# Kernel optimization log

Measured on AMD Instinct MI355X. Metric: run time of the kernel, lower is better.

## Reference

```python
import jax, jax.numpy as jnp
import numpy as np

N = 50000; E = 800000; F_IN = 128; H = 16; G = 256
DIMS = [F_IN, H, 2 * H, 4 * H, 4 * H, 8 * H]
EPS = 1e-5


def setup_inputs() -> dict:
    key = jax.random.key(0)
    ks = iter(jax.random.split(key, 40))
    inp = {}
    inp["x"] = jax.random.normal(next(ks), (N, F_IN), dtype=jnp.float32)
    inp["edge_index"] = jax.random.randint(next(ks), (2, E), 0, N, dtype=jnp.int32)
    inp["edge_weight"] = jax.random.uniform(next(ks), (E,), dtype=jnp.float32)
    inp["batch"] = jnp.sort(jax.random.randint(next(ks), (N,), 0, G, dtype=jnp.int32))
    for i in range(5):
        din, dout = DIMS[i], DIMS[i + 1]
        inp[f"W{i+1}"] = jax.random.normal(next(ks), (din, dout), dtype=jnp.float32) / np.sqrt(din).astype(np.float32)
        inp[f"b{i+1}"] = jnp.zeros((dout,), jnp.float32)
        inp[f"g{i+1}"] = jnp.ones((dout,), jnp.float32)
        inp[f"bt{i+1}"] = jnp.zeros((dout,), jnp.float32)
    inp["fc1_w"] = jax.random.normal(next(ks), (8 * H, 4 * H), dtype=jnp.float32) / np.sqrt(8 * H).astype(np.float32)
    inp["fc1_b"] = jnp.zeros((4 * H,), jnp.float32)
    inp["fc2_w"] = jax.random.normal(next(ks), (4 * H, 1), dtype=jnp.float32) / np.sqrt(4 * H).astype(np.float32)
    inp["fc2_b"] = jnp.zeros((1,), jnp.float32)
    return inp


def _gcn_norm(edge_index, edge_weight, n):
    # PyG GCNConv: add self-loops (weight 1), symmetric deg^-1/2 normalization.
    loop = jnp.arange(n, dtype=edge_index.dtype)
    row = jnp.concatenate([edge_index[0], loop])  # source
    col = jnp.concatenate([edge_index[1], loop])  # target
    w = jnp.concatenate([edge_weight, jnp.ones((n,), edge_weight.dtype)])
    deg = jax.ops.segment_sum(w, col, num_segments=n)
    dis = jnp.where(deg > 0, jax.lax.rsqrt(jnp.maximum(deg, 1e-12)), 0.0)
    return row, col, dis[row] * w * dis[col]


def _bn(h, g, b):
    # BatchNorm1d, training-mode batch statistics (biased variance, eps=1e-5)
    mu = h.mean(0)
    v = h.var(0)
    return g * (h - mu) * jax.lax.rsqrt(v + EPS) + b


def reference(x, edge_index, edge_weight, batch,
              W1, b1, g1, bt1, W2, b2, g2, bt2, W3, b3, g3, bt3,
              W4, b4, g4, bt4, W5, b5, g5, bt5,
              fc1_w, fc1_b, fc2_w, fc2_b):
    n = x.shape[0]
    row, col, norm = _gcn_norm(edge_index, edge_weight, n)

    def conv(h, W, b):
        m = h @ W                                   # [N, dout] dense transform
        agg = jax.ops.segment_sum(m[row] * norm[:, None], col, num_segments=n)
        return agg + b

    h = _bn(jax.nn.relu(conv(x, W1, b1)), g1, bt1)
    h = _bn(jax.nn.relu(conv(h, W2, b2)), g2, bt2)
    h = _bn(jax.nn.relu(conv(h, W3, b3)), g3, bt3)
    h = jax.nn.relu(_bn(conv(h, W4, b4), g4, bt4))   # layer4: conv->bn->relu
    h = _bn(conv(h, W5, b5), g5, bt5)                # layer5: conv->bn
    pooled = jax.ops.segment_sum(h, batch, num_segments=G)  # global_add_pool -> [G, 8H]
    p = jax.nn.relu(pooled)
    p = jax.nn.relu(p @ fc1_w + fc1_b)
    # dropout is identity in eval mode
    return (p @ fc2_w + fc2_b).reshape(-1)          # [G]
```

## Files before the change

kernel.cpp:

```cpp
#include <hip/hip_runtime.h>

#define NN 50000
#define NE 800000
#define NG 256
#define NBUCKET 16
#define PARTSZ (NBUCKET * 256)

#define NBKT 391
#define ABLK 391
#define ASLICE 2048
#define BCAP 2560

__device__ __forceinline__ float bf2f(unsigned short u) {
    return __uint_as_float(((unsigned)u) << 16);
}
__device__ __forceinline__ unsigned short f2bf(float f) {
    unsigned b = __float_as_uint(f);
    return (unsigned short)((b + 0x7FFF + ((b >> 16) & 1)) >> 16);
}

__global__ void k_init(float* part) {
    int i = blockIdx.x * blockDim.x + threadIdx.x;
    if (i < 5 * PARTSZ) part[i] = 0.f;
}

__global__ void kA1(const int* __restrict__ col, int* __restrict__ bb, int e) {
    __shared__ int cnt[NBKT];
    for (int j = threadIdx.x; j < NBKT; j += 256) cnt[j] = 0;
    __syncthreads();
    int start = blockIdx.x * ASLICE;
    int end = min(start + ASLICE, e);
    for (int i = start + threadIdx.x; i < end; i += 256)
        atomicAdd(&cnt[col[i] >> 7], 1);
    __syncthreads();
    for (int j = threadIdx.x; j < NBKT; j += 256) bb[blockIdx.x * NBKT + j] = cnt[j];
}

__global__ void kA2a(int* __restrict__ bb, int* __restrict__ totals) {
    __shared__ int v[ABLK];
    int k = blockIdx.x;
    for (int b = threadIdx.x; b < ABLK; b += 256) v[b] = bb[b * NBKT + k];
    __syncthreads();
    if (threadIdx.x == 0) {
        int run = 0;
        for (int b = 0; b < ABLK; ++b) { int t = v[b]; v[b] = run; run += t; }
        totals[k] = run;
    }
    __syncthreads();
    for (int b = threadIdx.x; b < ABLK; b += 256) bb[b * NBKT + k] = v[b];
}

__global__ void kA2b(const int* __restrict__ totals, int* __restrict__ bucketbase) {
    __shared__ int v[NBKT];
    for (int j = threadIdx.x; j < NBKT; j += 256) v[j] = totals[j];
    __syncthreads();
    if (threadIdx.x == 0) {
        int run = 0;
        for (int k = 0; k < NBKT; ++k) { int t = v[k]; v[k] = run; run += t; }
        bucketbase[NBKT] = run;
    }
    __syncthreads();
    for (int j = threadIdx.x; j < NBKT; j += 256) bucketbase[j] = v[j];
}

__global__ void kA3(const int* __restrict__ row, const int* __restrict__ col,
                    const float* __restrict__ ew, const int* __restrict__ bb,
                    const int* __restrict__ bucketbase, int2* __restrict__ staging, int e) {
    __shared__ int cur[NBKT];
    for (int j = threadIdx.x; j < NBKT; j += 256)
        cur[j] = bucketbase[j] + bb[blockIdx.x * NBKT + j];
    __syncthreads();
    int start = blockIdx.x * ASLICE;
    int end = min(start + ASLICE, e);
    for (int i = start + threadIdx.x; i < end; i += 256) {
        int c = col[i];
        int p = atomicAdd(&cur[c >> 7], 1);
        staging[p] = make_int2(row[i] | ((c & 127) << 16), __float_as_int(ew[i]));
    }
}

__global__ void __launch_bounds__(256) kB(const int* __restrict__ bucketbase,
                                          const int2* __restrict__ staging,
                                          int2* __restrict__ csr, int* __restrict__ ptr,
                                          float* __restrict__ dis, int n) {
    __shared__ int2 st[BCAP];
    __shared__ int2 outb[BCAP];
    __shared__ int hist[129];
    __shared__ int cur[128];
    int k = blockIdx.x, t = threadIdx.x;
    int base = bucketbase[k], cnt = bucketbase[k + 1] - base;
    int node0 = k << 7;
    int ncov = min(128, n - node0);
    if (t < 129) hist[t] = 0;
    __syncthreads();
    if (cnt <= BCAP) {
        for (int i = t; i < cnt; i += 256) {
            int2 v = staging[base + i];
            st[i] = v;
            atomicAdd(&hist[v.x >> 16], 1);
        }
        __syncthreads();
        if (t == 0) {
            int run = 0;
            for (int j = 0; j < 128; ++j) { int h = hist[j]; hist[j] = run; run += h; }
            hist[128] = run;
        }
        __syncthreads();
        if (t < 128) cur[t] = hist[t];
        if (t < ncov) ptr[node0 + t] = base + hist[t];
        __syncthreads();
        for (int i = t; i < cnt; i += 256) {
            int2 v = st[i];
            int j = v.x >> 16;
            int p = atomicAdd(&cur[j], 1);
            outb[p] = make_int2(v.x & 0xFFFF, v.y);
        }
        __syncthreads();
        for (int i = t; i < cnt; i += 256) csr[base + i] = outb[i];
        if (t < ncov) {
            float s = 1.f;
            int a = hist[t], b2 = hist[t + 1];
            for (int p = a; p < b2; ++p) s += __int_as_float(outb[p].y);
            dis[node0 + t] = rsqrtf(s);
        }
    } else {
        for (int i = t; i < cnt; i += 256) atomicAdd(&hist[staging[base + i].x >> 16], 1);
        __syncthreads();
        if (t == 0) {
            int run = 0;
            for (int j = 0; j < 128; ++j) { int h = hist[j]; hist[j] = run; run += h; }
            hist[128] = run;
        }
        __syncthreads();
        if (t < 128) cur[t] = hist[t];
        if (t < ncov) ptr[node0 + t] = base + hist[t];
        __syncthreads();
        for (int i = t; i < cnt; i += 256) {
            int2 v = staging[base + i];
            int j = v.x >> 16;
            int p = atomicAdd(&cur[j], 1);
            csr[base + p] = make_int2(v.x & 0xFFFF, v.y);
        }
        __threadfence_block();
        __syncthreads();
        if (t < ncov) {
            float s = 1.f;
            int a = hist[t], b2 = hist[t + 1];
            for (int p = a; p < b2; ++p) s += __int_as_float(csr[base + p].y);
            dis[node0 + t] = rsqrtf(s);
        }
    }
    if (k == gridDim.x - 1 && t == 0) ptr[n] = bucketbase[NBKT];
}

__global__ void k_scale(const int* __restrict__ ptr, int2* __restrict__ csr,
                        const float* __restrict__ dis, int n) {
    int i = blockIdx.x * blockDim.x + threadIdx.x;
    if (i >= n) return;
    float dc = dis[i];
    int p1 = ptr[i + 1];
    for (int p = ptr[i]; p < p1; ++p) {
        int2 v = csr[p];
        v.y = __float_as_int(dis[v.x] * __int_as_float(v.y) * dc);
        csr[p] = v;
    }
}

template <int D, int BF16>
__device__ __forceinline__ float4 load_row(const void* src, int node, int l4) {
    if (BF16) {
        const unsigned short* sb = (const unsigned short*)src;
        ushort4 r = *(const ushort4*)(sb + (size_t)node * D + (l4 << 2));
        float4 f;
        f.x = bf2f(r.x); f.y = bf2f(r.y); f.z = bf2f(r.z); f.w = bf2f(r.w);
        return f;
    } else {
        const float4* s4 = (const float4*)src;
        return s4[(size_t)node * (D / 4) + l4];
    }
}

template <int D, int EP, int POSTAFF, int PREAFF, int EPI, int BF16IN>
__global__ void k_gather(const void* __restrict__ src, const int* __restrict__ ptr,
                         const int2* __restrict__ csr, const float* __restrict__ dis,
                         const float* __restrict__ partIn, const float* __restrict__ gmv,
                         const float* __restrict__ btv,
                         const float* __restrict__ bias, float* __restrict__ partOut,
                         float* __restrict__ out, int n) {
    const int TPN = D / 4;
    const int LPN = TPN * EP;
    const int CONSUME = POSTAFF || PREAFF;
    __shared__ float ls[EPI ? D : 1], lq[EPI ? D : 1];
    __shared__ float scs[CONSUME ? D : 4], shs[CONSUME ? D : 4];
    int tid = threadIdx.x;
    if (EPI && tid < D) { ls[tid] = 0.f; lq[tid] = 0.f; }
    if (CONSUME && tid < D) {
        float s = 0.f, q = 0.f;
#pragma unroll
        for (int b2 = 0; b2 < NBUCKET; ++b2) {
            s += partIn[b2 * 256 + tid];
            q += partIn[b2 * 256 + 128 + tid];
        }
        float mu = s / (float)n;
        float var = q / (float)n - mu * mu;
        float a = gmv[tid] * rsqrtf(var + 1e-5f);
        scs[tid] = a;
        shs[tid] = btv[tid] - mu * a;
    }
    if (EPI || CONSUME) __syncthreads();

    int t = blockIdx.x * blockDim.x + tid;
    int node = t / LPN;
    int r = t - node * LPN;
    int e0 = r / TPN;
    int l4 = r - e0 * TPN;
    bool valid = node < n;
    int nc = valid ? node : n - 1;

    float4 sc = {0,0,0,0}, sh = {0,0,0,0};
    if (CONSUME) {
        sc = ((const float4*)scs)[l4];
        sh = ((const float4*)shs)[l4];
    }
    float4 acc = {0.f, 0.f, 0.f, 0.f};
    float sumw = 0.f;
    if (e0 == 0) {
        float d = dis[nc];
        float w0 = d * d;
        float4 v = load_row<D, BF16IN>(src, nc, l4);
        if (PREAFF) {
            v.x = fmaxf(sc.x * v.x + sh.x, 0.f); v.y = fmaxf(sc.y * v.y + sh.y, 0.f);
            v.z = fmaxf(sc.z * v.z + sh.z, 0.f); v.w = fmaxf(sc.w * v.w + sh.w, 0.f);
        }
        acc.x = w0 * v.x; acc.y = w0 * v.y; acc.z = w0 * v.z; acc.w = w0 * v.w;
        sumw = w0;
    }
    int p0 = ptr[nc], p1 = ptr[nc + 1];
    int p = p0 + e0;
    for (; p + 3 * EP < p1; p += 4 * EP) {
        int2 c0 = csr[p], c1 = csr[p + EP], c2 = csr[p + 2 * EP], c3 = csr[p + 3 * EP];
        float e0w = __int_as_float(c0.y), e1w = __int_as_float(c1.y);
        float e2w = __int_as_float(c2.y), e3w = __int_as_float(c3.y);
        float4 u0 = load_row<D, BF16IN>(src, c0.x, l4);
        float4 u1 = load_row<D, BF16IN>(src, c1.x, l4);
        float4 u2 = load_row<D, BF16IN>(src, c2.x, l4);
        float4 u3 = load_row<D, BF16IN>(src, c3.x, l4);
        if (PREAFF) {
            u0.x = fmaxf(sc.x*u0.x+sh.x,0.f); u0.y = fmaxf(sc.y*u0.y+sh.y,0.f);
            u0.z = fmaxf(sc.z*u0.z+sh.z,0.f); u0.w = fmaxf(sc.w*u0.w+sh.w,0.f);
            u1.x = fmaxf(sc.x*u1.x+sh.x,0.f); u1.y = fmaxf(sc.y*u1.y+sh.y,0.f);
            u1.z = fmaxf(sc.z*u1.z+sh.z,0.f); u1.w = fmaxf(sc.w*u1.w+sh.w,0.f);
            u2.x = fmaxf(sc.x*u2.x+sh.x,0.f); u2.y = fmaxf(sc.y*u2.y+sh.y,0.f);
            u2.z = fmaxf(sc.z*u2.z+sh.z,0.f); u2.w = fmaxf(sc.w*u2.w+sh.w,0.f);
            u3.x = fmaxf(sc.x*u3.x+sh.x,0.f); u3.y = fmaxf(sc.y*u3.y+sh.y,0.f);
            u3.z = fmaxf(sc.z*u3.z+sh.z,0.f); u3.w = fmaxf(sc.w*u3.w+sh.w,0.f);
        }
        acc.x += e0w*u0.x + e1w*u1.x + e2w*u2.x + e3w*u3.x;
        acc.y += e0w*u0.y + e1w*u1.y + e2w*u2.y + e3w*u3.y;
        acc.z += e0w*u0.z + e1w*u1.z + e2w*u2.z + e3w*u3.z;
        acc.w += e0w*u0.w + e1w*u1.w + e2w*u2.w + e3w*u3.w;
        if (POSTAFF) sumw += e0w + e1w + e2w + e3w;
    }
    for (; p < p1; p += EP) {
        int2 ce = csr[p];
        float w = __int_as_float(ce.y);
        float4 u = load_row<D, BF16IN>(src, ce.x, l4);
        if (PREAFF) {
            u.x = fmaxf(sc.x*u.x+sh.x,0.f); u.y = fmaxf(sc.y*u.y+sh.y,0.f);
            u.z = fmaxf(sc.z*u.z+sh.z,0.f); u.w = fmaxf(sc.w*u.w+sh.w,0.f);
        }
        acc.x += w*u.x; acc.y += w*u.y; acc.z += w*u.z; acc.w += w*u.w;
        if (POSTAFF) sumw += w;
    }
    if (EP > 1) {
#pragma unroll
        for (int off = TPN; off < LPN; off <<= 1) {
            acc.x += __shfl_xor(acc.x, off, 64);
            acc.y += __shfl_xor(acc.y, off, 64);
            acc.z += __shfl_xor(acc.z, off, 64);
            acc.w += __shfl_xor(acc.w, off, 64);
            if (POSTAFF) sumw += __shfl_xor(sumw, off, 64);
        }
    }
    if (POSTAFF) {
        acc.x = sc.x * acc.x + sh.x * sumw;
        acc.y = sc.y * acc.y + sh.y * sumw;
        acc.z = sc.z * acc.z + sh.z * sumw;
        acc.w = sc.w * acc.w + sh.w * sumw;
    }
    if (EPI) {
        float4 b = ((const float4*)bias)[l4];
        acc.x = fmaxf(acc.x + b.x, 0.f);
        acc.y = fmaxf(acc.y + b.y, 0.f);
        acc.z = fmaxf(acc.z + b.z, 0.f);
        acc.w = fmaxf(acc.w + b.w, 0.f);
        if (valid) ((float4*)out)[nc * TPN + l4] = acc;
        float s0 = valid ? acc.x : 0.f, s1 = valid ? acc.y : 0.f;
        float s2 = valid ? acc.z : 0.f, s3 = valid ? acc.w : 0.f;
        float q0 = s0*s0, q1 = s1*s1, q2 = s2*s2, q3 = s3*s3;
        for (int off = TPN; off < 64; off <<= 1) {
            s0 += __shfl_down(s0, off, 64); s1 += __shfl_down(s1, off, 64);
            s2 += __shfl_down(s2, off, 64); s3 += __shfl_down(s3, off, 64);
            q0 += __shfl_down(q0, off, 64); q1 += __shfl_down(q1, off, 64);
            q2 += __shfl_down(q2, off, 64); q3 += __shfl_down(q3, off, 64);
        }
        int lane = tid & 63;
        if (lane < TPN) {
            atomicAdd(&ls[4*lane+0], s0); atomicAdd(&ls[4*lane+1], s1);
            atomicAdd(&ls[4*lane+2], s2); atomicAdd(&ls[4*lane+3], s3);
            atomicAdd(&lq[4*lane+0], q0); atomicAdd(&lq[4*lane+1], q1);
            atomicAdd(&lq[4*lane+2], q2); atomicAdd(&lq[4*lane+3], q3);
        }
        __syncthreads();
        int bkt = (blockIdx.x & (NBUCKET - 1)) * 256;
        if (tid < D) {
            atomicAdd(&partOut[bkt + tid], ls[tid]);
            atomicAdd(&partOut[bkt + 128 + tid], lq[tid]);
        }
    } else {
        if (valid && e0 == 0) ((float4*)out)[nc * TPN + l4] = acc;
    }
}

template <int DIN, int DOUT, int RELU, int EPI, int NPT, int BF16OUT>
__global__ void k_gemm(const float* __restrict__ h, const float* __restrict__ W,
                       const float* __restrict__ bias, float* __restrict__ partOut,
                       void* __restrict__ m, int n) {
    const int TPN = DOUT / 4;
    const int GPB = 256 / TPN;
    __shared__ float Wl[DIN * DOUT];
    __shared__ float ls[EPI ? DOUT : 1], lq[EPI ? DOUT : 1];
    int tid = threadIdx.x;
    for (int i = tid; i < DIN * DOUT / 4; i += 256)
        ((float4*)Wl)[i] = ((const float4*)W)[i];
    if (EPI && tid < DOUT) { ls[tid] = 0.f; lq[tid] = 0.f; }
    __syncthreads();

    int jq = tid % TPN;
    int group = tid / TPN;
    int node0 = (blockIdx.x * GPB + group) * NPT;
    const float4* h4 = (const float4*)h;
    int hb[NPT];
    bool val[NPT];
#pragma unroll
    for (int i = 0; i < NPT; ++i) {
        int nd = node0 + i;
        val[i] = nd < n;
        hb[i] = (val[i] ? nd : n - 1) * (DIN / 4);
    }
    float4 acc[NPT];
#pragma unroll
    for (int i = 0; i < NPT; ++i) acc[i] = {0.f, 0.f, 0.f, 0.f};

#pragma unroll 4
    for (int k4 = 0; k4 < DIN / 4; ++k4) {
        const float* wb = &Wl[(k4 * 4) * DOUT + jq * 4];
        float4 w0 = *(const float4*)(wb);
        float4 w1 = *(const float4*)(wb + DOUT);
        float4 w2 = *(const float4*)(wb + 2 * DOUT);
        float4 w3 = *(const float4*)(wb + 3 * DOUT);
#pragma unroll
        for (int i = 0; i < NPT; ++i) {
            float4 hv = h4[hb[i] + k4];
            acc[i].x += hv.x*w0.x + hv.y*w1.x + hv.z*w2.x + hv.w*w3.x;
            acc[i].y += hv.x*w0.y + hv.y*w1.y + hv.z*w2.y + hv.w*w3.y;
            acc[i].z += hv.x*w0.z + hv.y*w1.z + hv.z*w2.z + hv.w*w3.z;
            acc[i].w += hv.x*w0.w + hv.y*w1.w + hv.z*w2.w + hv.w*w3.w;
        }
    }

    float4 bv = {0,0,0,0};
    if (EPI) bv = ((const float4*)bias)[jq];
    float4 sv = {0,0,0,0}, qv = {0,0,0,0};
#pragma unroll
    for (int i = 0; i < NPT; ++i) {
        float4 a = acc[i];
        if (EPI) {
            a.x += bv.x; a.y += bv.y; a.z += bv.z; a.w += bv.w;
            if (RELU) {
                a.x = fmaxf(a.x, 0.f); a.y = fmaxf(a.y, 0.f);
                a.z = fmaxf(a.z, 0.f); a.w = fmaxf(a.w, 0.f);
            }
        }
        if (val[i]) {
            if (BF16OUT) {
                ushort4 o;
                o.x = f2bf(a.x); o.y = f2bf(a.y); o.z = f2bf(a.z); o.w = f2bf(a.w);
                *(ushort4*)((unsigned short*)m + (size_t)(node0 + i) * DOUT + (jq << 2)) = o;
            } else {
                ((float4*)m)[(size_t)(node0 + i) * TPN + jq] = a;
            }
            if (EPI) {
                sv.x += a.x; sv.y += a.y; sv.z += a.z; sv.w += a.w;
                qv.x += a.x*a.x; qv.y += a.y*a.y; qv.z += a.z*a.z; qv.w += a.w*a.w;
            }
        }
    }
    if (EPI) {
        for (int off = TPN; off < 64; off <<= 1) {
            sv.x += __shfl_down(sv.x, off, 64); sv.y += __shfl_down(sv.y, off, 64);
            sv.z += __shfl_down(sv.z, off, 64); sv.w += __shfl_down(sv.w, off, 64);
            qv.x += __shfl_down(qv.x, off, 64); qv.y += __shfl_down(qv.y, off, 64);
            qv.z += __shfl_down(qv.z, off, 64); qv.w += __shfl_down(qv.w, off, 64);
        }
        int lane = tid & 63;
        if (lane < TPN) {
            atomicAdd(&ls[4*lane+0], sv.x); atomicAdd(&ls[4*lane+1], sv.y);
            atomicAdd(&ls[4*lane+2], sv.z); atomicAdd(&ls[4*lane+3], sv.w);
            atomicAdd(&lq[4*lane+0], qv.x); atomicAdd(&lq[4*lane+1], qv.y);
            atomicAdd(&lq[4*lane+2], qv.z); atomicAdd(&lq[4*lane+3], qv.w);
        }
        __syncthreads();
        int bkt = (blockIdx.x & (NBUCKET - 1)) * 256;
        if (tid < DOUT) {
            atomicAdd(&partOut[bkt + tid], ls[tid]);
            atomicAdd(&partOut[bkt + 128 + tid], lq[tid]);
        }
    }
}

__global__ void k_poolhead(const float* __restrict__ h, const int* __restrict__ batch,
                           const float* __restrict__ partIn, const float* __restrict__ gmv,
                           const float* __restrict__ btv,
                           const float* __restrict__ fc1w, const float* __restrict__ fc1b,
                           const float* __restrict__ fc2w, const float* __restrict__ fc2b,
                           float* __restrict__ out, int n) {
    __shared__ float tmp[256];
    __shared__ float pl[128];
    __shared__ float scs[128], shs[128];
    int g = blockIdx.x;
    int tid = threadIdx.x;
    if (tid < 128) {
        float s = 0.f, q = 0.f;
#pragma unroll
        for (int b2 = 0; b2 < NBUCKET; ++b2) {
            s += partIn[b2 * 256 + tid];
            q += partIn[b2 * 256 + 128 + tid];
        }
        float mu = s / (float)n;
        float var = q / (float)n - mu * mu;
        float a = gmv[tid] * rsqrtf(var + 1e-5f);
        scs[tid] = a;
        shs[tid] = btv[tid] - mu * a;
    }
    int j = tid & 127, prt = tid >> 7;
    int a = 0, b = n;
    while (a < b) { int mid = (a + b) >> 1; if (batch[mid] < g) a = mid + 1; else b = mid; }
    int lo = a;
    b = n;
    while (a < b) { int mid = (a + b) >> 1; if (batch[mid] < g + 1) a = mid + 1; else b = mid; }
    int hi = a;

    float acc = 0.f;
    for (int node = lo + prt; node < hi; node += 2) acc += h[(long)node * 128 + j];
    tmp[tid] = acc;
    __syncthreads();
    if (tid < 128) {
        float cnt = (float)(hi - lo);
        float p = scs[tid] * (tmp[tid] + tmp[tid + 128]) + shs[tid] * cnt;
        pl[tid] = fmaxf(p, 0.f);
    }
    __syncthreads();
    if (tid < 64) {
        float v1 = fc1b[tid];
        for (int k = 0; k < 128; ++k) v1 += pl[k] * fc1w[k * 64 + tid];
        v1 = fmaxf(v1, 0.f);
        float v = v1 * fc2w[tid];
        for (int off = 32; off > 0; off >>= 1) v += __shfl_down(v, off, 64);
        if (tid == 0) out[g] = v + fc2b[0];
    }
}

extern "C" void kernel_launch(void* const* d_in, const int* in_sizes, int n_in,
                              void* d_out, int out_size, void* d_ws, size_t ws_size,
                              hipStream_t stream) {
    const float* x     = (const float*)d_in[0];
    const int*   ei    = (const int*)d_in[1];
    const float* ew    = (const float*)d_in[2];
    const int*   batch = (const int*)d_in[3];
    const float *W[5], *b[5], *gm[5], *bt[5];
    for (int i = 0; i < 5; ++i) {
        W[i]  = (const float*)d_in[4 + 4 * i];
        b[i]  = (const float*)d_in[5 + 4 * i];
        gm[i] = (const float*)d_in[6 + 4 * i];
        bt[i] = (const float*)d_in[7 + 4 * i];
    }
    const float* fc1w = (const float*)d_in[24];
    const float* fc1b = (const float*)d_in[25];
    const float* fc2w = (const float*)d_in[26];
    const float* fc2b = (const float*)d_in[27];
    float* out = (float*)d_out;

    char* wsb = (char*)d_ws;
    float* dis    = (float*)wsb;  wsb += sizeof(float) * NN;
    int*   ptr    = (int*)wsb;    wsb += sizeof(int) * (NN + 4);
    int*   bb     = (int*)wsb;    wsb += sizeof(int) * ABLK * NBKT;
    int*   totals = (int*)wsb;    wsb += sizeof(int) * (NBKT + 1);
    int*   bbase  = (int*)wsb;    wsb += sizeof(int) * (NBKT + 3);
    int2*  staging= (int2*)wsb;   wsb += sizeof(int2) * NE;
    int2*  csr    = (int2*)wsb;   wsb += sizeof(int2) * NE;
    float* part   = (float*)wsb;  wsb += sizeof(float) * 5 * PARTSZ;
    unsigned short* bufB = (unsigned short*)wsb;  wsb += sizeof(unsigned short) * (size_t)NN * 64;
    float* buf1   = (float*)wsb;  wsb += sizeof(float) * (long)NN * 128;
    float* buf2   = (float*)wsb;  wsb += sizeof(float) * (long)NN * 128;

    const int* row = ei;
    const int* col = ei + NE;
    const int B = 256;
    const int NB_N = (NN + B - 1) / B;

    k_init<<<(5 * PARTSZ + B - 1) / B, B, 0, stream>>>(part);
    kA1<<<ABLK, B, 0, stream>>>(col, bb, NE);
    kA2a<<<NBKT, B, 0, stream>>>(bb, totals);
    kA2b<<<1, B, 0, stream>>>(totals, bbase);
    kA3<<<ABLK, B, 0, stream>>>(row, col, ew, bb, bbase, staging, NE);
    kB<<<NBKT, B, 0, stream>>>(bbase, staging, csr, ptr, dis, NN);
    k_scale<<<NB_N, B, 0, stream>>>(ptr, csr, dis, NN);

    auto grid4 = [](long threads) { return (int)((threads + 255) / 256); };
    auto ggrid = [](int npb) { return (NN + npb - 1) / npb; };

    k_gemm<128, 16, 0, 0, 2, 0><<<ggrid((256/4)*2), B, 0, stream>>>(x, W[0], b[0], nullptr, buf1, NN);
    k_gather<16, 1, 0, 0, 1, 0><<<grid4((long)NN * 4), B, 0, stream>>>(buf1, ptr, csr, dis,
                                                                       nullptr, nullptr, nullptr,
                                                                       b[0], part + 0 * PARTSZ, buf2, NN);

    k_gather<16, 1, 1, 0, 0, 0><<<grid4((long)NN * 4), B, 0, stream>>>(buf2, ptr, csr, dis,
                                                                       part + 0 * PARTSZ, gm[0], bt[0],
                                                                       nullptr, nullptr, buf1, NN);
    k_gemm<16, 32, 1, 1, 4, 1><<<ggrid((256/8)*4), B, 0, stream>>>(buf1, W[1], b[1], part + 1 * PARTSZ, bufB, NN);

    k_gather<32, 4, 1, 0, 0, 1><<<grid4((long)NN * 32), B, 0, stream>>>(bufB, ptr, csr, dis,
                                                                        part + 1 * PARTSZ, gm[1], bt[1],
                                                                        nullptr, nullptr, buf1, NN);
    k_gemm<32, 64, 1, 1, 4, 1><<<ggrid((256/16)*4), B, 0, stream>>>(buf1, W[2], b[2], part + 2 * PARTSZ, bufB, NN);

    k_gather<64, 4, 1, 0, 0, 1><<<grid4((long)NN * 64), B, 0, stream>>>(bufB, ptr, csr, dis,
                                                                        part + 2 * PARTSZ, gm[2], bt[2],
                                                                        nullptr, nullptr, buf1, NN);
    k_gemm<64, 64, 0, 1, 4, 1><<<ggrid((256/16)*4), B, 0, stream>>>(buf1, W[3], b[3], part + 3 * PARTSZ, bufB, NN);

    k_gather<64, 4, 0, 1, 0, 1><<<grid4((long)NN * 64), B, 0, stream>>>(bufB, ptr, csr, dis,
                                                                        part + 3 * PARTSZ, gm[3], bt[3],
                                                                        nullptr, nullptr, buf1, NN);
    k_gemm<64, 128, 0, 1, 4, 0><<<ggrid((256/32)*4), B, 0, stream>>>(buf1, W[4], b[4], part + 4 * PARTSZ, buf2, NN);

    k_poolhead<<<NG, 256, 0, stream>>>(buf2, batch, part + 4 * PARTSZ, gm[4], bt[4],
                                       fc1w, fc1b, fc2w, fc2b, out, NN);
}
```

Measured before the change: 426.0 us.

## Fuse gather and dense transform per layer, fold edge scaling into first gather

Layers 2-5 now run as one kernel each: a block aggregates 16 nodes' neighbour rows into shared memory, then applies the weight matrix from shared memory, so the intermediate aggregated features no longer round-trip through global memory. The separate edge-weight normalisation pass is folded into the first-layer gather, which writes the normalised weights back into the CSR array. Zeroing of the statistics buffer moves into the histogram kernel, removing two launches. The trade-off is 16-node blocks with a large shared weight tile, which may lower occupancy and repeat the weight load in every block.

```diff
diff --git a/kernel.cpp b/kernel.cpp
--- a/kernel.cpp
+++ b/kernel.cpp
@@ -1,4 +1,5 @@
 #include <hip/hip_runtime.h>
+#include <stdint.h>
 
 #define NN 50000
 #define NE 800000
@@ -19,14 +20,10 @@
     return (unsigned short)((b + 0x7FFF + ((b >> 16) & 1)) >> 16);
 }
 
-__global__ void k_init(float* part) {
-    int i = blockIdx.x * blockDim.x + threadIdx.x;
-    if (i < 5 * PARTSZ) part[i] = 0.f;
-}
-
-__global__ void kA1(const int* __restrict__ col, int* __restrict__ bb, int e) {
+__global__ void kA1(const int* __restrict__ col, int* __restrict__ bb, float* part, int e) {
     __shared__ int cnt[NBKT];
     for (int j = threadIdx.x; j < NBKT; j += 256) cnt[j] = 0;
+    for (int i = blockIdx.x * 256 + threadIdx.x; i < 5 * PARTSZ; i += ABLK * 256) part[i] = 0.f;
     __syncthreads();
     int start = blockIdx.x * ASLICE;
     int end = min(start + ASLICE, e);
@@ -153,16 +150,121 @@
     if (k == gridDim.x - 1 && t == 0) ptr[n] = bucketbase[NBKT];
 }
 
-__global__ void k_scale(const int* __restrict__ ptr, int2* __restrict__ csr,
-                        const float* __restrict__ dis, int n) {
-    int i = blockIdx.x * blockDim.x + threadIdx.x;
-    if (i >= n) return;
-    float dc = dis[i];
-    int p1 = ptr[i + 1];
-    for (int p = ptr[i]; p < p1; ++p) {
-        int2 v = csr[p];
-        v.y = __float_as_int(dis[v.x] * __int_as_float(v.y) * dc);
-        csr[p] = v;
+__global__ void k_gemm1(const float* __restrict__ h, const float* __restrict__ W,
+                        float* __restrict__ m, int n) {
+    __shared__ float Wl[128 * 16];
+    int tid = threadIdx.x;
+    for (int i = tid; i < 128 * 16 / 4; i += 256)
+        ((float4*)Wl)[i] = ((const float4*)W)[i];
+    __syncthreads();
+    int jq = tid % 4, group = tid / 4;
+    int node0 = (blockIdx.x * 64 + group) * 2;
+    const float4* h4 = (const float4*)h;
+    int hb[2]; bool val[2];
+#pragma unroll
+    for (int i = 0; i < 2; ++i) {
+        int nd = node0 + i;
+        val[i] = nd < n;
+        hb[i] = (val[i] ? nd : n - 1) * 32;
+    }
+    float4 acc[2];
+    acc[0] = {0,0,0,0}; acc[1] = {0,0,0,0};
+#pragma unroll 4
+    for (int k4 = 0; k4 < 32; ++k4) {
+        const float* wb = &Wl[(k4 * 4) * 16 + jq * 4];
+        float4 w0 = *(const float4*)(wb);
+        float4 w1 = *(const float4*)(wb + 16);
+        float4 w2 = *(const float4*)(wb + 32);
+        float4 w3 = *(const float4*)(wb + 48);
+#pragma unroll
+        for (int i = 0; i < 2; ++i) {
+            float4 hv = h4[hb[i] + k4];
+            acc[i].x += hv.x*w0.x + hv.y*w1.x + hv.z*w2.x + hv.w*w3.x;
+            acc[i].y += hv.x*w0.y + hv.y*w1.y + hv.z*w2.y + hv.w*w3.y;
+            acc[i].z += hv.x*w0.z + hv.y*w1.z + hv.z*w2.z + hv.w*w3.z;
+            acc[i].w += hv.x*w0.w + hv.y*w1.w + hv.z*w2.w + hv.w*w3.w;
+        }
+    }
+#pragma unroll
+    for (int i = 0; i < 2; ++i)
+        if (val[i]) ((float4*)m)[(node0 + i) * 4 + jq] = acc[i];
+}
+
+__global__ void k_l1gather(const float* __restrict__ src, const int* __restrict__ ptr,
+                           int2* __restrict__ csr, const float* __restrict__ dis,
+                           const float* __restrict__ bias, float* __restrict__ partOut,
+                           float* __restrict__ out, int n) {
+    __shared__ float ls[16], lq[16];
+    int tid = threadIdx.x;
+    if (tid < 16) { ls[tid] = 0.f; lq[tid] = 0.f; }
+    __syncthreads();
+    int t = blockIdx.x * 256 + tid;
+    int node = t >> 2;
+    int l4 = t & 3;
+    bool valid = node < n;
+    int nc = valid ? node : n - 1;
+    const float4* s4 = (const float4*)src;
+    float dc = dis[nc];
+    float w0 = dc * dc;
+    float4 v = s4[nc * 4 + l4];
+    float4 acc = { w0 * v.x, w0 * v.y, w0 * v.z, w0 * v.w };
+    int p0 = ptr[nc], p1 = ptr[nc + 1];
+    int p = p0;
+    for (; p + 4 <= p1; p += 4) {
+        int2 c0 = csr[p], c1 = csr[p+1], c2 = csr[p+2], c3 = csr[p+3];
+        float e0 = dis[c0.x] * __int_as_float(c0.y) * dc;
+        float e1 = dis[c1.x] * __int_as_float(c1.y) * dc;
+        float e2 = dis[c2.x] * __int_as_float(c2.y) * dc;
+        float e3 = dis[c3.x] * __int_as_float(c3.y) * dc;
+        float4 u0 = s4[c0.x * 4 + l4];
+        float4 u1 = s4[c1.x * 4 + l4];
+        float4 u2 = s4[c2.x * 4 + l4];
+        float4 u3 = s4[c3.x * 4 + l4];
+        acc.x += e0*u0.x + e1*u1.x + e2*u2.x + e3*u3.x;
+        acc.y += e0*u0.y + e1*u1.y + e2*u2.y + e3*u3.y;
+        acc.z += e0*u0.z + e1*u1.z + e2*u2.z + e3*u3.z;
+        acc.w += e0*u0.w + e1*u1.w + e2*u2.w + e3*u3.w;
+        if (l4 == 0) {
+            csr[p]   = make_int2(c0.x, __float_as_int(e0));
+            csr[p+1] = make_int2(c1.x, __float_as_int(e1));
+            csr[p+2] = make_int2(c2.x, __float_as_int(e2));
+            csr[p+3] = make_int2(c3.x, __float_as_int(e3));
+        }
+    }
+    for (; p < p1; ++p) {
+        int2 ce = csr[p];
+        float w = dis[ce.x] * __int_as_float(ce.y) * dc;
+        float4 u = s4[ce.x * 4 + l4];
+        acc.x += w*u.x; acc.y += w*u.y; acc.z += w*u.z; acc.w += w*u.w;
+        if (l4 == 0) csr[p] = make_int2(ce.x, __float_as_int(w));
+    }
+    float4 b = ((const float4*)bias)[l4];
+    acc.x = fmaxf(acc.x + b.x, 0.f);
+    acc.y = fmaxf(acc.y + b.y, 0.f);
+    acc.z = fmaxf(acc.z + b.z, 0.f);
+    acc.w = fmaxf(acc.w + b.w, 0.f);
+    if (valid) ((float4*)out)[nc * 4 + l4] = acc;
+    float s0 = valid ? acc.x : 0.f, s1 = valid ? acc.y : 0.f;
+    float s2 = valid ? acc.z : 0.f, s3 = valid ? acc.w : 0.f;
+    float q0 = s0*s0, q1 = s1*s1, q2 = s2*s2, q3 = s3*s3;
+    for (int off = 4; off < 64; off <<= 1) {
+        s0 += __shfl_down(s0, off, 64); s1 += __shfl_down(s1, off, 64);
+        s2 += __shfl_down(s2, off, 64); s3 += __shfl_down(s3, off, 64);
+        q0 += __shfl_down(q0, off, 64); q1 += __shfl_down(q1, off, 64);
+        q2 += __shfl_down(q2, off, 64); q3 += __shfl_down(q3, off, 64);
+    }
+    int lane = tid & 63;
+    if (lane < 4) {
+        atomicAdd(&ls[4*lane+0], s0); atomicAdd(&ls[4*lane+1], s1);
+        atomicAdd(&ls[4*lane+2], s2); atomicAdd(&ls[4*lane+3], s3);
+        atomicAdd(&lq[4*lane+0], q0); atomicAdd(&lq[4*lane+1], q1);
+        atomicAdd(&lq[4*lane+2], q2); atomicAdd(&lq[4*lane+3], q3);
+    }
+    __syncthreads();
+    int bkt = (blockIdx.x & (NBUCKET - 1)) * 256;
+    if (tid < 16) {
+        atomicAdd(&partOut[bkt + tid], ls[tid]);
+        atomicAdd(&partOut[bkt + 128 + tid], lq[tid]);
     }
 }
 
@@ -180,21 +282,26 @@
     }
 }
 
-template <int D, int EP, int POSTAFF, int PREAFF, int EPI, int BF16IN>
-__global__ void k_gather(const void* __restrict__ src, const int* __restrict__ ptr,
-                         const int2* __restrict__ csr, const float* __restrict__ dis,
-                         const float* __restrict__ partIn, const float* __restrict__ gmv,
-                         const float* __restrict__ btv,
-                         const float* __restrict__ bias, float* __restrict__ partOut,
-                         float* __restrict__ out, int n) {
-    const int TPN = D / 4;
-    const int LPN = TPN * EP;
-    const int CONSUME = POSTAFF || PREAFF;
-    __shared__ float ls[EPI ? D : 1], lq[EPI ? D : 1];
-    __shared__ float scs[CONSUME ? D : 4], shs[CONSUME ? D : 4];
+template <int DIN, int DOUT, int EP, int POSTAFF, int PREAFF, int RELU,
+          int BF16IN, int BF16OUT, int NPB>
+__global__ void __launch_bounds__(256) k_fused(
+        const void* __restrict__ src, const int* __restrict__ ptr,
+        const int2* __restrict__ csr, const float* __restrict__ dis,
+        const float* __restrict__ partIn, const float* __restrict__ gmv,
+        const float* __restrict__ btv, const float* __restrict__ W,
+        const float* __restrict__ bias, float* __restrict__ partOut,
+        void* __restrict__ out, int n) {
+    const int TPN1 = DIN / 4, LPN = TPN1 * EP, GN1 = 256 / LPN;
+    const int TPN2 = DOUT / 4, G2 = 256 / TPN2;
+    const int HS = DIN + 4;
+    __shared__ float Wl[DIN * DOUT];
+    __shared__ float hrow[NPB * HS];
+    __shared__ float scs[DIN], shs[DIN];
+    __shared__ float ls[DOUT], lq[DOUT];
     int tid = threadIdx.x;
-    if (EPI && tid < D) { ls[tid] = 0.f; lq[tid] = 0.f; }
-    if (CONSUME && tid < D) {
+    for (int i = tid; i < DIN * DOUT / 4; i += 256)
+        ((float4*)Wl)[i] = ((const float4*)W)[i];
+    if (tid < DIN) {
         float s = 0.f, q = 0.f;
 #pragma unroll
         for (int b2 = 0; b2 < NBUCKET; ++b2) {
@@ -207,204 +314,134 @@
         scs[tid] = a;
         shs[tid] = btv[tid] - mu * a;
     }
-    if (EPI || CONSUME) __syncthreads();
-
-    int t = blockIdx.x * blockDim.x + tid;
-    int node = t / LPN;
-    int r = t - node * LPN;
-    int e0 = r / TPN;
-    int l4 = r - e0 * TPN;
-    bool valid = node < n;
-    int nc = valid ? node : n - 1;
-
-    float4 sc = {0,0,0,0}, sh = {0,0,0,0};
-    if (CONSUME) {
-        sc = ((const float4*)scs)[l4];
-        sh = ((const float4*)shs)[l4];
-    }
-    float4 acc = {0.f, 0.f, 0.f, 0.f};
-    float sumw = 0.f;
-    if (e0 == 0) {
-        float d = dis[nc];
-        float w0 = d * d;
-        float4 v = load_row<D, BF16IN>(src, nc, l4);
-        if (PREAFF) {
-            v.x = fmaxf(sc.x * v.x + sh.x, 0.f); v.y = fmaxf(sc.y * v.y + sh.y, 0.f);
-            v.z = fmaxf(sc.z * v.z + sh.z, 0.f); v.w = fmaxf(sc.w * v.w + sh.w, 0.f);
-        }
-        acc.x = w0 * v.x; acc.y = w0 * v.y; acc.z = w0 * v.z; acc.w = w0 * v.w;
-        sumw = w0;
-    }
-    int p0 = ptr[nc], p1 = ptr[nc + 1];
-    int p = p0 + e0;
-    for (; p + 3 * EP < p1; p += 4 * EP) {
-        int2 c0 = csr[p], c1 = csr[p + EP], c2 = csr[p + 2 * EP], c3 = csr[p + 3 * EP];
-        float e0w = __int_as_float(c0.y), e1w = __int_as_float(c1.y);
-        float e2w = __int_as_float(c2.y), e3w = __int_as_float(c3.y);
-        float4 u0 = load_row<D, BF16IN>(src, c0.x, l4);
-        float4 u1 = load_row<D, BF16IN>(src, c1.x, l4);
-        float4 u2 = load_row<D, BF16IN>(src, c2.x, l4);
-        float4 u3 = load_row<D, BF16IN>(src, c3.x, l4);
-        if (PREAFF) {
-            u0.x = fmaxf(sc.x*u0.x+sh.x,0.f); u0.y = fmaxf(sc.y*u0.y+sh.y,0.f);
-            u0.z = fmaxf(sc.z*u0.z+sh.z,0.f); u0.w = fmaxf(sc.w*u0.w+sh.w,0.f);
-            u1.x = fmaxf(sc.x*u1.x+sh.x,0.f); u1.y = fmaxf(sc.y*u1.y+sh.y,0.f);
-            u1.z = fmaxf(sc.z*u1.z+sh.z,0.f); u1.w = fmaxf(sc.w*u1.w+sh.w,0.f);
-            u2.x = fmaxf(sc.x*u2.x+sh.x,0.f); u2.y = fmaxf(sc.y*u2.y+sh.y,0.f);
-            u2.z = fmaxf(sc.z*u2.z+sh.z,0.f); u2.w = fmaxf(sc.w*u2.w+sh.w,0.f);
-            u3.x = fmaxf(sc.x*u3.x+sh.x,0.f); u3.y = fmaxf(sc.y*u3.y+sh.y,0.f);
-            u3.z = fmaxf(sc.z*u3.z+sh.z,0.f); u3.w = fmaxf(sc.w*u3.w+sh.w,0.f);
-        }
-        acc.x += e0w*u0.x + e1w*u1.x + e2w*u2.x + e3w*u3.x;
-        acc.y += e0w*u0.y + e1w*u1.y + e2w*u2.y + e3w*u3.y;
-        acc.z += e0w*u0.z + e1w*u1.z + e2w*u2.z + e3w*u3.z;
-        acc.w += e0w*u0.w + e1w*u1.w + e2w*u2.w + e3w*u3.w;
-        if (POSTAFF) sumw += e0w + e1w + e2w + e3w;
-    }
-    for (; p < p1; p += EP) {
-        int2 ce = csr[p];
-        float w = __int_as_float(ce.y);
-        float4 u = load_row<D, BF16IN>(src, ce.x, l4);
-        if (PREAFF) {
-            u.x = fmaxf(sc.x*u.x+sh.x,0.f); u.y = fmaxf(sc.y*u.y+sh.y,0.f);
-            u.z = fmaxf(sc.z*u.z+sh.z,0.f); u.w = fmaxf(sc.w*u.w+sh.w,0.f);
-        }
-        acc.x += w*u.x; acc.y += w*u.y; acc.z += w*u.z; acc.w += w*u.w;
-        if (POSTAFF) sumw += w;
-    }
-    if (EP > 1) {
-#pragma unroll
-        for (int off = TPN; off < LPN; off <<= 1) {
-            acc.x += __shfl_xor(acc.x, off, 64);
-            acc.y += __shfl_xor(acc.y, off, 64);
-            acc.z += __shfl_xor(acc.z, off, 64);
-            acc.w += __shfl_xor(acc.w, off, 64);
-            if (POSTAFF) sumw += __shfl_xor(sumw, off, 64);
-        }
-    }
-    if (POSTAFF) {
-        acc.x = sc.x * acc.x + sh.x * sumw;
-        acc.y = sc.y * acc.y + sh.y * sumw;
-        acc.z = sc.z * acc.z + sh.z * sumw;
-        acc.w = sc.w * acc.w + sh.w * sumw;
-    }
-    if (EPI) {
-        float4 b = ((const float4*)bias)[l4];
-        acc.x = fmaxf(acc.x + b.x, 0.f);
-        acc.y = fmaxf(acc.y + b.y, 0.f);
-        acc.z = fmaxf(acc.z + b.z, 0.f);
-        acc.w = fmaxf(acc.w + b.w, 0.f);
-        if (valid) ((float4*)out)[nc * TPN + l4] = acc;
-        float s0 = valid ? acc.x : 0.f, s1 = valid ? acc.y : 0.f;
-        float s2 = valid ? acc.z : 0.f, s3 = valid ? acc.w : 0.f;
-        float q0 = s0*s0, q1 = s1*s1, q2 = s2*s2, q3 = s3*s3;
-        for (int off = TPN; off < 64; off <<= 1) {
-            s0 += __shfl_down(s0, off, 64); s1 += __shfl_down(s1, off, 64);
-            s2 += __shfl_down(s2, off, 64); s3 += __shfl_down(s3, off, 64);
-            q0 += __shfl_down(q0, off, 64); q1 += __shfl_down(q1, off, 64);
-            q2 += __shfl_down(q2, off, 64); q3 += __shfl_down(q3, off, 64);
-        }
-        int lane = tid & 63;
-        if (lane < TPN) {
-            atomicAdd(&ls[4*lane+0], s0); atomicAdd(&ls[4*lane+1], s1);
-            atomicAdd(&ls[4*lane+2], s2); atomicAdd(&ls[4*lane+3], s3);
-            atomicAdd(&lq[4*lane+0], q0); atomicAdd(&lq[4*lane+1], q1);
-            atomicAdd(&lq[4*lane+2], q2); atomicAdd(&lq[4*lane+3], q3);
-        }
-        __syncthreads();
-        int bkt = (blockIdx.x & (NBUCKET - 1)) * 256;
-        if (tid < D) {
-            atomicAdd(&partOut[bkt + tid], ls[tid]);
-            atomicAdd(&partOut[bkt + 128 + tid], lq[tid]);
-        }
-    } else {
-        if (valid && e0 == 0) ((float4*)out)[nc * TPN + l4] = acc;
-    }
-}
-
-template <int DIN, int DOUT, int RELU, int EPI, int NPT, int BF16OUT>
-__global__ void k_gemm(const float* __restrict__ h, const float* __restrict__ W,
-                       const float* __restrict__ bias, float* __restrict__ partOut,
-                       void* __restrict__ m, int n) {
-    const int TPN = DOUT / 4;
-    const int GPB = 256 / TPN;
-    __shared__ float Wl[DIN * DOUT];
-    __shared__ float ls[EPI ? DOUT : 1], lq[EPI ? DOUT : 1];
-    int tid = threadIdx.x;
-    for (int i = tid; i < DIN * DOUT / 4; i += 256)
-        ((float4*)Wl)[i] = ((const float4*)W)[i];
-    if (EPI && tid < DOUT) { ls[tid] = 0.f; lq[tid] = 0.f; }
-    __syncthreads();
-
-    int jq = tid % TPN;
-    int group = tid / TPN;
-    int node0 = (blockIdx.x * GPB + group) * NPT;
-    const float4* h4 = (const float4*)h;
-    int hb[NPT];
-    bool val[NPT];
-#pragma unroll
-    for (int i = 0; i < NPT; ++i) {
-        int nd = node0 + i;
-        val[i] = nd < n;
-        hb[i] = (val[i] ? nd : n - 1) * (DIN / 4);
-    }
-    float4 acc[NPT];
-#pragma unroll
-    for (int i = 0; i < NPT; ++i) acc[i] = {0.f, 0.f, 0.f, 0.f};
-
-#pragma unroll 4
-    for (int k4 = 0; k4 < DIN / 4; ++k4) {
-        const float* wb = &Wl[(k4 * 4) * DOUT + jq * 4];
-        float4 w0 = *(const float4*)(wb);
-        float4 w1 = *(const float4*)(wb + DOUT);
-        float4 w2 = *(const float4*)(wb + 2 * DOUT);
-        float4 w3 = *(const float4*)(wb + 3 * DOUT);
-#pragma unroll
-        for (int i = 0; i < NPT; ++i) {
-            float4 hv = h4[hb[i] + k4];
-            acc[i].x += hv.x*w0.x + hv.y*w1.x + hv.z*w2.x + hv.w*w3.x;
-            acc[i].y += hv.x*w0.y + hv.y*w1.y + hv.z*w2.y + hv.w*w3.y;
-            acc[i].z += hv.x*w0.z + hv.y*w1.z + hv.z*w2.z + hv.w*w3.z;
-            acc[i].w += hv.x*w0.w + hv.y*w1.w + hv.z*w2.w + hv.w*w3.w;
-        }
-    }
-
-    float4 bv = {0,0,0,0};
-    if (EPI) bv = ((const float4*)bias)[jq];
-    float4 sv = {0,0,0,0}, qv = {0,0,0,0};
-#pragma unroll
-    for (int i = 0; i < NPT; ++i) {
-        float4 a = acc[i];
-        if (EPI) {
+    if (tid < DOUT) { ls[tid] = 0.f; lq[tid] = 0.f; }
+    __syncthreads();
+
+    int nodebase = blockIdx.x * NPB;
+    {
+        int grp = tid / LPN, r = tid % LPN;
+        int e0 = r / TPN1, l4 = r % TPN1;
+        float4 sc = ((const float4*)scs)[l4];
+        float4 sh = ((const float4*)shs)[l4];
+#pragma unroll
+        for (int pass = 0; pass < NPB / GN1; ++pass) {
+            int nl = pass * GN1 + grp;
+            int node = nodebase + nl;
+            int nc = node < n ? node : n - 1;
+            float4 acc = {0.f, 0.f, 0.f, 0.f};
+            float sumw = 0.f;
+            if (e0 == 0) {
+                float d = dis[nc];
+                float w0 = d * d;
+                float4 v = load_row<DIN, BF16IN>(src, nc, l4);
+                if (PREAFF) {
+                    v.x = fmaxf(sc.x*v.x+sh.x, 0.f); v.y = fmaxf(sc.y*v.y+sh.y, 0.f);
+                    v.z = fmaxf(sc.z*v.z+sh.z, 0.f); v.w = fmaxf(sc.w*v.w+sh.w, 0.f);
+                }
+                acc.x = w0*v.x; acc.y = w0*v.y; acc.z = w0*v.z; acc.w = w0*v.w;
+                sumw = w0;
+            }
+            int p0 = ptr[nc], p1 = ptr[nc + 1];
+            int p = p0 + e0;
+            for (; p + 3 * EP < p1; p += 4 * EP) {
+                int2 c0 = csr[p], c1 = csr[p + EP], c2 = csr[p + 2*EP], c3 = csr[p + 3*EP];
+                float e0w = __int_as_float(c0.y), e1w = __int_as_float(c1.y);
+                float e2w = __int_as_float(c2.y), e3w = __int_as_float(c3.y);
+                float4 u0 = load_row<DIN, BF16IN>(src, c0.x, l4);
+                float4 u1 = load_row<DIN, BF16IN>(src, c1.x, l4);
+                float4 u2 = load_row<DIN, BF16IN>(src, c2.x, l4);
+                float4 u3 = load_row<DIN, BF16IN>(src, c3.x, l4);
+                if (PREAFF) {
+                    u0.x = fmaxf(sc.x*u0.x+sh.x,0.f); u0.y = fmaxf(sc.y*u0.y+sh.y,0.f);
+                    u0.z = fmaxf(sc.z*u0.z+sh.z,0.f); u0.w = fmaxf(sc.w*u0.w+sh.w,0.f);
+                    u1.x = fmaxf(sc.x*u1.x+sh.x,0.f); u1.y = fmaxf(sc.y*u1.y+sh.y,0.f);
+                    u1.z = fmaxf(sc.z*u1.z+sh.z,0.f); u1.w = fmaxf(sc.w*u1.w+sh.w,0.f);
+                    u2.x = fmaxf(sc.x*u2.x+sh.x,0.f); u2.y = fmaxf(sc.y*u2.y+sh.y,0.f);
+                    u2.z = fmaxf(sc.z*u2.z+sh.z,0.f); u2.w = fmaxf(sc.w*u2.w+sh.w,0.f);
+                    u3.x = fmaxf(sc.x*u3.x+sh.x,0.f); u3.y = fmaxf(sc.y*u3.y+sh.y,0.f);
+                    u3.z = fmaxf(sc.z*u3.z+sh.z,0.f); u3.w = fmaxf(sc.w*u3.w+sh.w,0.f);
+                }
+                acc.x += e0w*u0.x + e1w*u1.x + e2w*u2.x + e3w*u3.x;
+                acc.y += e0w*u0.y + e1w*u1.y + e2w*u2.y + e3w*u3.y;
+                acc.z += e0w*u0.z + e1w*u1.z + e2w*u2.z + e3w*u3.z;
+                acc.w += e0w*u0.w + e1w*u1.w + e2w*u2.w + e3w*u3.w;
+                if (POSTAFF) sumw += e0w + e1w + e2w + e3w;
+            }
+            for (; p < p1; p += EP) {
+                int2 ce = csr[p];
+                float w = __int_as_float(ce.y);
+                float4 u = load_row<DIN, BF16IN>(src, ce.x, l4);
+                if (PREAFF) {
+                    u.x = fmaxf(sc.x*u.x+sh.x,0.f); u.y = fmaxf(sc.y*u.y+sh.y,0.f);
+                    u.z = fmaxf(sc.z*u.z+sh.z,0.f); u.w = fmaxf(sc.w*u.w+sh.w,0.f);
+                }
+                acc.x += w*u.x; acc.y += w*u.y; acc.z += w*u.z; acc.w += w*u.w;
+                if (POSTAFF) sumw += w;
+            }
+#pragma unroll
+            for (int off = TPN1; off < LPN; off <<= 1) {
+                acc.x += __shfl_xor(acc.x, off, 64);
+                acc.y += __shfl_xor(acc.y, off, 64);
+                acc.z += __shfl_xor(acc.z, off, 64);
+                acc.w += __shfl_xor(acc.w, off, 64);
+                if (POSTAFF) sumw += __shfl_xor(sumw, off, 64);
+            }
+            if (POSTAFF) {
+                acc.x = sc.x * acc.x + sh.x * sumw;
+                acc.y = sc.y * acc.y + sh.y * sumw;
+                acc.z = sc.z * acc.z + sh.z * sumw;
+                acc.w = sc.w * acc.w + sh.w * sumw;
+            }
+            if (e0 == 0) *(float4*)&hrow[nl * HS + (l4 << 2)] = acc;
+        }
+    }
+    __syncthreads();
+    {
+        int jq = tid % TPN2, g2 = tid / TPN2;
+        float4 bv = ((const float4*)bias)[jq];
+        float4 sv = {0,0,0,0}, qv = {0,0,0,0};
+        for (int nl = g2; nl < NPB; nl += G2) {
+            int node = nodebase + nl;
+            bool valid = node < n;
+            float4 a = {0.f, 0.f, 0.f, 0.f};
+#pragma unroll
+            for (int k4 = 0; k4 < DIN / 4; ++k4) {
+                float4 hv = *(const float4*)&hrow[nl * HS + (k4 << 2)];
+                const float* wb = &Wl[(k4 * 4) * DOUT + jq * 4];
+                float4 w0 = *(const float4*)(wb);
+                float4 w1 = *(const float4*)(wb + DOUT);
+                float4 w2 = *(const float4*)(wb + 2 * DOUT);
+                float4 w3 = *(const float4*)(wb + 3 * DOUT);
+                a.x += hv.x*w0.x + hv.y*w1.x + hv.z*w2.x + hv.w*w3.x;
+                a.y += hv.x*w0.y + hv.y*w1.y + hv.z*w2.y + hv.w*w3.y;
+                a.z += hv.x*w0.z + hv.y*w1.z + hv.z*w2.z + hv.w*w3.z;
+                a.w += hv.x*w0.w + hv.y*w1.w + hv.z*w2.w + hv.w*w3.w;
+            }
             a.x += bv.x; a.y += bv.y; a.z += bv.z; a.w += bv.w;
             if (RELU) {
                 a.x = fmaxf(a.x, 0.f); a.y = fmaxf(a.y, 0.f);
                 a.z = fmaxf(a.z, 0.f); a.w = fmaxf(a.w, 0.f);
             }
-        }
-        if (val[i]) {
-            if (BF16OUT) {
-                ushort4 o;
-                o.x = f2bf(a.x); o.y = f2bf(a.y); o.z = f2bf(a.z); o.w = f2bf(a.w);
-                *(ushort4*)((unsigned short*)m + (size_t)(node0 + i) * DOUT + (jq << 2)) = o;
-            } else {
-                ((float4*)m)[(size_t)(node0 + i) * TPN + jq] = a;
-            }
-            if (EPI) {
+            if (valid) {
+                if (BF16OUT) {
+                    ushort4 o;
+                    o.x = f2bf(a.x); o.y = f2bf(a.y); o.z = f2bf(a.z); o.w = f2bf(a.w);
+                    *(ushort4*)((unsigned short*)out + (size_t)node * DOUT + (jq << 2)) = o;
+                } else {
+                    ((float4*)out)[(size_t)node * TPN2 + jq] = a;
+                }
                 sv.x += a.x; sv.y += a.y; sv.z += a.z; sv.w += a.w;
                 qv.x += a.x*a.x; qv.y += a.y*a.y; qv.z += a.z*a.z; qv.w += a.w*a.w;
             }
         }
-    }
-    if (EPI) {
-        for (int off = TPN; off < 64; off <<= 1) {
+        for (int off = TPN2; off < 64; off <<= 1) {
             sv.x += __shfl_down(sv.x, off, 64); sv.y += __shfl_down(sv.y, off, 64);
             sv.z += __shfl_down(sv.z, off, 64); sv.w += __shfl_down(sv.w, off, 64);
             qv.x += __shfl_down(qv.x, off, 64); qv.y += __shfl_down(qv.y, off, 64);
             qv.z += __shfl_down(qv.z, off, 64); qv.w += __shfl_down(qv.w, off, 64);
         }
         int lane = tid & 63;
-        if (lane < TPN) {
+        if (lane < TPN2) {
             atomicAdd(&ls[4*lane+0], sv.x); atomicAdd(&ls[4*lane+1], sv.y);
             atomicAdd(&ls[4*lane+2], sv.z); atomicAdd(&ls[4*lane+3], sv.w);
             atomicAdd(&lq[4*lane+0], qv.x); atomicAdd(&lq[4*lane+1], qv.y);
@@ -497,54 +534,43 @@
     int*   bb     = (int*)wsb;    wsb += sizeof(int) * ABLK * NBKT;
     int*   totals = (int*)wsb;    wsb += sizeof(int) * (NBKT + 1);
     int*   bbase  = (int*)wsb;    wsb += sizeof(int) * (NBKT + 3);
+    wsb = (char*)(((uintptr_t)wsb + 15) & ~(uintptr_t)15);
     int2*  staging= (int2*)wsb;   wsb += sizeof(int2) * NE;
     int2*  csr    = (int2*)wsb;   wsb += sizeof(int2) * NE;
     float* part   = (float*)wsb;  wsb += sizeof(float) * 5 * PARTSZ;
-    unsigned short* bufB = (unsigned short*)wsb;  wsb += sizeof(unsigned short) * (size_t)NN * 64;
-    float* buf1   = (float*)wsb;  wsb += sizeof(float) * (long)NN * 128;
-    float* buf2   = (float*)wsb;  wsb += sizeof(float) * (long)NN * 128;
+    unsigned short* bufB1 = (unsigned short*)wsb;  wsb += sizeof(unsigned short) * (size_t)NN * 64;
+    unsigned short* bufB2 = (unsigned short*)wsb;  wsb += sizeof(unsigned short) * (size_t)NN * 64;
+    float* buf1   = (float*)wsb;  wsb += sizeof(float) * (size_t)NN * 16;
+    float* buf2   = (float*)wsb;  wsb += sizeof(float) * (size_t)NN * 128;
 
     const int* row = ei;
     const int* col = ei + NE;
     const int B = 256;
-    const int NB_N = (NN + B - 1) / B;
-
-    k_init<<<(5 * PARTSZ + B - 1) / B, B, 0, stream>>>(part);
-    kA1<<<ABLK, B, 0, stream>>>(col, bb, NE);
+    const int NBF = (NN + 15) / 16;
+
+    kA1<<<ABLK, B, 0, stream>>>(col, bb, part, NE);
     kA2a<<<NBKT, B, 0, stream>>>(bb, totals);
     kA2b<<<1, B, 0, stream>>>(totals, bbase);
     kA3<<<ABLK, B, 0, stream>>>(row, col, ew, bb, bbase, staging, NE);
     kB<<<NBKT, B, 0, stream>>>(bbase, staging, csr, ptr, dis, NN);
-    k_scale<<<NB_N, B, 0, stream>>>(ptr, csr, dis, NN);
-
-    auto grid4 = [](long threads) { return (int)((threads + 255) / 256); };
-    auto ggrid = [](int npb) { return (NN + npb - 1) / npb; };
-
-    k_gemm<128, 16, 0, 0, 2, 0><<<ggrid((256/4)*2), B, 0, stream>>>(x, W[0], b[0], nullptr, buf1, NN);
-    k_gather<16, 1, 0, 0, 1, 0><<<grid4((long)NN * 4), B, 0, stream>>>(buf1, ptr, csr, dis,
-                                                                       nullptr, nullptr, nullptr,
-                                                                       b[0], part + 0 * PARTSZ, buf2, NN);
-
-    k_gather<16, 1, 1, 0, 0, 0><<<grid4((long)NN * 4), B, 0, stream>>>(buf2, ptr, csr, dis,
-                                                                       part + 0 * PARTSZ, gm[0], bt[0],
-                                                                       nullptr, nullptr, buf1, NN);
-    k_gemm<16, 32, 1, 1, 4, 1><<<ggrid((256/8)*4), B, 0, stream>>>(buf1, W[1], b[1], part + 1 * PARTSZ, bufB, NN);
-
-    k_gather<32, 4, 1, 0, 0, 1><<<grid4((long)NN * 32), B, 0, stream>>>(bufB, ptr, csr, dis,
-                                                                        part + 1 * PARTSZ, gm[1], bt[1],
-                                                                        nullptr, nullptr, buf1, NN);
-    k_gemm<32, 64, 1, 1, 4, 1><<<ggrid((256/16)*4), B, 0, stream>>>(buf1, W[2], b[2], part + 2 * PARTSZ, bufB, NN);
-
-    k_gather<64, 4, 1, 0, 0, 1><<<grid4((long)NN * 64), B, 0, stream>>>(bufB, ptr, csr, dis,
-                                                                        part + 2 * PARTSZ, gm[2], bt[2],
-                                                                        nullptr, nullptr, buf1, NN);
-    k_gemm<64, 64, 0, 1, 4, 1><<<ggrid((256/16)*4), B, 0, stream>>>(buf1, W[3], b[3], part + 3 * PARTSZ, bufB, NN);
-
-    k_gather<64, 4, 0, 1, 0, 1><<<grid4((long)NN * 64), B, 0, stream>>>(bufB, ptr, csr, dis,
-                                                                        part + 3 * PARTSZ, gm[3], bt[3],
-                                                                        nullptr, nullptr, buf1, NN);
-    k_gemm<64, 128, 0, 1, 4, 0><<<ggrid((256/32)*4), B, 0, stream>>>(buf1, W[4], b[4], part + 4 * PARTSZ, buf2, NN);
-
-    k_poolhead<<<NG, 256, 0, stream>>>(buf2, batch, part + 4 * PARTSZ, gm[4], bt[4],
-                                       fc1w, fc1b, fc2w, fc2b, out, NN);
-}
+
+    k_gemm1<<<(NN + 127) / 128, B, 0, stream>>>(x, W[0], buf1, NN);
+    k_l1gather<<<(NN * 4 + 255) / 256, B, 0, stream>>>(buf1, ptr, csr, dis,
+                                                       b[0], part + 0 * PARTSZ, buf2, NN);
+
+    k_fused<16, 32, 4, 1, 0, 1, 0, 1, 16><<<NBF, B, 0, stream>>>(
+        buf2, ptr, csr, dis, part + 0 * PARTSZ, gm[0], bt[0],
+        W[1], b[1], part + 1 * PARTSZ, bufB1, NN);
+    k_fused<32, 64, 4, 1, 0, 1, 1, 1, 16><<<NBF, B, 0, stream>>>(
+        bufB1, ptr, csr, dis, part + 1 * PARTSZ, gm[1], bt[1],
+        W[2], b[2], part + 2 * PARTSZ, bufB2, NN);
+    k_fused<64, 64, 4, 1, 0, 0, 1, 1, 16><<<NBF, B, 0, stream>>>(
+        bufB2, ptr, csr, dis, part + 2 * PARTSZ, gm[2], bt[2],
+        W[3], b[3], part + 3 * PARTSZ, bufB1, NN);
+    k_fused<64, 128, 4, 0, 1, 0, 1, 0, 16><<<NBF, B, 0, stream>>>(
+        bufB1, ptr, csr, dis, part + 3 * PARTSZ, gm[3], bt[3],
+        W[4], b[4], part + 4 * PARTSZ, buf2, NN);
+
+    k_poolhead<<<NG, B, 0, stream>>>(buf2, batch, part + 4 * PARTSZ, gm[4], bt[4],
+                                     fc1w, fc1b, fc2w, fc2b, out, NN);
+}
```

Result: no change. 421.6 us (-1.0%).
